# Optimization experiments

Hardware: AMD Instinct MI355X
Metric: run time of the kernel (lower is better)

## Reference

```python
import jax, jax.numpy as jnp
import numpy as np

B, T, N, F_IN = 4, 8, 2048, 16
HID, HEADS, OUT_CH, OUT_FEAT = 128, 4, 64, 14
E = 32768


def _ln(x, g, b, eps=1e-5):
    mu = x.mean(-1, keepdims=True)
    var = ((x - mu) ** 2).mean(-1, keepdims=True)
    return (x - mu) / jnp.sqrt(var + eps) * g + b


def _attn_steps(x, wq, bq, wk, bk, wv, bv, wo, bo):
    # x: [B, S, M, F]; single-head causal attention over axis 1 (the 'steps' axis)
    q = x @ wq + bq
    k = x @ wk + bk
    v = x @ wv + bv
    scale = 1.0 / np.sqrt(q.shape[-1]).astype(np.float32)
    scores = jnp.einsum('bsmh,btmh->bmst', q, k) * scale  # [B,M,S,S]
    S = scores.shape[-1]
    scores = jnp.where(jnp.tril(jnp.ones((S, S), bool)), scores, -jnp.inf)
    a = jax.nn.softmax(scores, axis=-1)
    ctx = jnp.einsum('bmst,btmh->bsmh', a, v)
    return ctx @ wo + bo


def _attn_nodes(x, wq, bq, wk, bk, wv, bv, wo, bo):
    # single-head attention over axis 2 (the 'nodes' axis)
    q = x @ wq + bq
    k = x @ wk + bk
    v = x @ wv + bv
    scale = 1.0 / np.sqrt(q.shape[-1]).astype(np.float32)
    scores = jnp.einsum('bsnh,bsmh->bsnm', q, k) * scale
    a = jax.nn.softmax(scores, axis=-1)
    ctx = jnp.einsum('bsnm,bsmh->bsnh', a, v)
    return ctx @ wo + bo


def _gat(h, src, dst, n, W, a_src, a_dst, bias, heads, out_ch, concat):
    # PyG GATConv: gather src/dst features per edge, segment softmax over
    # incoming edges of each target node, weighted scatter-aggregate.
    hw = (h @ W).reshape(n, heads, out_ch)
    al_s = (hw * a_src).sum(-1)  # [n, heads]
    al_d = (hw * a_dst).sum(-1)
    loop = jnp.arange(n, dtype=src.dtype)
    src_f = jnp.concatenate([src, loop])
    dst_f = jnp.concatenate([dst, loop])
    alpha = jax.nn.leaky_relu(al_s[src_f] + al_d[dst_f], 0.2)
    # PyG removes pre-existing self-loops then adds canonical ones: mask them out.
    drop = jnp.concatenate([src == dst, jnp.zeros((n,), bool)])[:, None]
    amax = jax.lax.stop_gradient(
        jax.ops.segment_max(jnp.where(drop, -jnp.inf, alpha), dst_f, num_segments=n))
    ex = jnp.where(drop, 0.0, jnp.exp(alpha - amax[dst_f]))
    denom = jax.ops.segment_sum(ex, dst_f, num_segments=n)
    w = ex / denom[dst_f]  # [E_total, heads]
    out = jax.ops.segment_sum(hw[src_f] * w[:, :, None], dst_f, num_segments=n)
    if concat:
        return out.reshape(n, heads * out_ch) + bias
    return out.mean(1) + bias


def _forward(x, edge_index, ln1_g, ln1_b, t_wq, t_bq, t_wk, t_bk, t_wv, t_bv, t_wo, t_bo,
             skip_w, skip_b, ln2_g, ln2_b, s_wq, s_bq, s_wk, s_bk, s_wv, s_bv, s_wo, s_bo,
             ln3_g, ln3_b, mlp_w1, mlp_b1, mlp_w2, mlp_b2,
             gat1_w, gat1_asrc, gat1_adst, gat1_b, gat2_w, gat2_asrc, gat2_adst, gat2_b,
             ffn_w, ffn_b):
    Bx, Tx, Nx, _ = x.shape
    h = jnp.transpose(x, (0, 2, 1, 3))  # [B, N(steps), T(nodes), F]
    h = (h @ skip_w + skip_b) + _attn_steps(_ln(h, ln1_g, ln1_b),
                                            t_wq, t_bq, t_wk, t_bk, t_wv, t_bv, t_wo, t_bo)
    h = h + _attn_nodes(_ln(h, ln2_g, ln2_b), s_wq, s_bq, s_wk, s_bk, s_wv, s_bv, s_wo, s_bo)
    z = _ln(h, ln3_g, ln3_b)
    h = h + (jax.nn.relu(z @ mlp_w1 + mlp_b1) @ mlp_w2 + mlp_b2)
    h = h[:, :, -1, :].reshape(Bx * Nx, HID)  # last 'nodes'(=T) slot, flatten graphs
    src, dst = edge_index[0], edge_index[1]
    off = jnp.repeat(jnp.arange(Bx, dtype=src.dtype) * Nx, src.shape[0])
    src_b = jnp.tile(src, Bx) + off
    dst_b = jnp.tile(dst, Bx) + off
    nt = Bx * Nx
    g1 = jax.nn.elu(_gat(h, src_b, dst_b, nt, gat1_w, gat1_asrc, gat1_adst, gat1_b,
                         HEADS, HID // HEADS, True))
    g2 = _gat(g1, src_b, dst_b, nt, gat2_w, gat2_asrc, gat2_adst, gat2_b, 1, OUT_CH, False)
    out = g2.reshape(Bx, Nx, OUT_CH) @ ffn_w + ffn_b
    return jnp.transpose(out, (0, 2, 1))  # [B, output_features, N]


def setup_inputs():
    key = jax.random.key(0)
    ki = iter(list(jax.random.split(key, 40)))
    def rn(shape, s=0.05):
        return jax.random.normal(next(ki), shape, jnp.float32) * s
    d = {}
    d['x'] = jax.random.normal(next(ki), (B, T, N, F_IN), jnp.float32)
    d['edge_index'] = jax.random.randint(next(ki), (2, E), 0, N, jnp.int32)
    d['ln1_g'] = jnp.ones((F_IN,), jnp.float32); d['ln1_b'] = jnp.zeros((F_IN,), jnp.float32)
    d['t_wq'] = rn((F_IN, HID)); d['t_bq'] = jnp.zeros((HID,), jnp.float32)
    d['t_wk'] = rn((F_IN, HID)); d['t_bk'] = jnp.zeros((HID,), jnp.float32)
    d['t_wv'] = rn((F_IN, HID)); d['t_bv'] = jnp.zeros((HID,), jnp.float32)
    d['t_wo'] = rn((HID, HID)); d['t_bo'] = jnp.zeros((HID,), jnp.float32)
    d['skip_w'] = rn((F_IN, HID)); d['skip_b'] = jnp.zeros((HID,), jnp.float32)
    d['ln2_g'] = jnp.ones((HID,), jnp.float32); d['ln2_b'] = jnp.zeros((HID,), jnp.float32)
    d['s_wq'] = rn((HID, HID)); d['s_bq'] = jnp.zeros((HID,), jnp.float32)
    d['s_wk'] = rn((HID, HID)); d['s_bk'] = jnp.zeros((HID,), jnp.float32)
    d['s_wv'] = rn((HID, HID)); d['s_bv'] = jnp.zeros((HID,), jnp.float32)
    d['s_wo'] = rn((HID, HID)); d['s_bo'] = jnp.zeros((HID,), jnp.float32)
    d['ln3_g'] = jnp.ones((HID,), jnp.float32); d['ln3_b'] = jnp.zeros((HID,), jnp.float32)
    d['mlp_w1'] = rn((HID, 2 * HID)); d['mlp_b1'] = jnp.zeros((2 * HID,), jnp.float32)
    d['mlp_w2'] = rn((2 * HID, HID)); d['mlp_b2'] = jnp.zeros((HID,), jnp.float32)
    d['gat1_w'] = rn((HID, HID))
    d['gat1_asrc'] = rn((HEADS, HID // HEADS)); d['gat1_adst'] = rn((HEADS, HID // HEADS))
    d['gat1_b'] = jnp.zeros((HID,), jnp.float32)
    d['gat2_w'] = rn((HID, OUT_CH))
    d['gat2_asrc'] = rn((1, OUT_CH)); d['gat2_adst'] = rn((1, OUT_CH))
    d['gat2_b'] = jnp.zeros((OUT_CH,), jnp.float32)
    d['ffn_w'] = rn((OUT_CH, OUT_FEAT)); d['ffn_b'] = jnp.zeros((OUT_FEAT,), jnp.float32)
    return d


def reference(x, edge_index, ln1_g, ln1_b, t_wq, t_bq, t_wk, t_bk, t_wv, t_bv, t_wo, t_bo,
              skip_w, skip_b, ln2_g, ln2_b, s_wq, s_bq, s_wk, s_bk, s_wv, s_bv, s_wo, s_bo,
              ln3_g, ln3_b, mlp_w1, mlp_b1, mlp_w2, mlp_b2,
              gat1_w, gat1_asrc, gat1_adst, gat1_b, gat2_w, gat2_asrc, gat2_adst, gat2_b,
              ffn_w, ffn_b):
    return _forward(x, edge_index, ln1_g, ln1_b, t_wq, t_bq, t_wk, t_bk, t_wv, t_bv, t_wo, t_bo,
                    skip_w, skip_b, ln2_g, ln2_b, s_wq, s_bq, s_wk, s_bk, s_wv, s_bv, s_wo, s_bo,
                    ln3_g, ln3_b, mlp_w1, mlp_b1, mlp_w2, mlp_b2,
                    gat1_w, gat1_asrc, gat1_adst, gat1_b, gat2_w, gat2_asrc, gat2_adst, gat2_b,
                    ffn_w, ffn_b)
```

## Files before the change

### kernel.cpp

```cpp
#include <hip/hip_runtime.h>
#include <hip/hip_bf16.h>
#include <stdint.h>


#define BB     4
#define TT     8
#define NN     2048
#define FIN    16
#define HID    128
#define BM     (BB*TT)
#define PROWS  (BM*NN)
#define NHEADS 4
#define OUTCH  64
#define OUTF   14
#define NEDGE  32768
#define NEDGEB (NEDGE*BB)
#define NNODE  (BB*NN)
#define NETOT  (NEDGEB + NNODE)

#define TQ     64
#define NTILE  (NN/TQ)

typedef __hip_bfloat16 bf16;
typedef __attribute__((ext_vector_type(8))) short bf16x8;
typedef __attribute__((ext_vector_type(4))) float f32x4;

__device__ __forceinline__ float b2f(bf16 v){ return __bfloat162float(v); }
__device__ __forceinline__ bf16  f2b(float f){ return __float2bfloat16(f); }
__device__ __forceinline__ unsigned short bfbits(float f){
    union { bf16 h; unsigned short u; } cv; cv.h = f2b(f); return cv.u;
}

__global__ __launch_bounds__(256)
void k_kv(const float* __restrict__ x,
          const float* __restrict__ g1, const float* __restrict__ bb1,
          const float* __restrict__ wk, const float* __restrict__ bk,
          const float* __restrict__ wv, const float* __restrict__ bv,
          int in_off, bf16* __restrict__ K, bf16* __restrict__ Vt)
{
    const int r0 = blockIdx.x * 32;
    const int t  = threadIdx.x;

    __shared__ float wk_s[FIN][HID];
    __shared__ float wv_s[FIN][HID];
    __shared__ float xr_s[32][FIN+1];
    __shared__ float ln_s[32][FIN+1];

    #pragma unroll
    for (int it = 0; it < 2; ++it){
        const int u = t + it*256;
        ((float4*)wk_s)[u] = ((const float4*)wk)[u];
        ((float4*)wv_s)[u] = ((const float4*)wv)[u];
    }
    #pragma unroll
    for (int it = 0; it < 2; ++it){
        const int u = t + it*256;
        xr_s[u >> 4][u & 15] = x[(size_t)(r0 + in_off)*FIN + u];
    }
    __syncthreads();

    if (t < 32){
        float mu = 0.f;
        #pragma unroll
        for (int f = 0; f < FIN; ++f) mu += xr_s[t][f];
        mu *= (1.f/FIN);
        float var = 0.f;
        #pragma unroll
        for (int f = 0; f < FIN; ++f){ float d = xr_s[t][f]-mu; var += d*d; }
        var *= (1.f/FIN);
        const float inv = rsqrtf(var + 1e-5f);
        #pragma unroll
        for (int f = 0; f < FIN; ++f)
            ln_s[t][f] = (xr_s[t][f]-mu)*inv*g1[f] + bb1[f];
    }
    __syncthreads();

    {
        const int hk = (t & 63)*2;
        const float2 bkv = *(const float2*)&bk[hk];
        #pragma unroll
        for (int pass = 0; pass < 8; ++pass){
            const int key = pass*4 + (t >> 6);
            float a0 = bkv.x, a1 = bkv.y;
            #pragma unroll
            for (int f = 0; f < FIN; ++f){
                const float l = ln_s[key][f];
                const float2 wkv = ((const float2*)&wk_s[f][0])[t & 63];
                a0 += l*wkv.x; a1 += l*wkv.y;
            }
            const unsigned int pk =
                (unsigned int)bfbits(a0) | ((unsigned int)bfbits(a1) << 16);
            *(unsigned int*)(void*)&K[((size_t)(r0 + key))*HID + hk] = pk;
        }
    }

    {
        const int slice = r0 >> 11;
        const int kg    = (r0 & (NN-1)) >> 5;
        const size_t vbase = ((size_t)slice*(NN/32) + kg)*(size_t)HID*32;
        const int kk = (t & 15)*2;
        #pragma unroll
        for (int pass = 0; pass < 8; ++pass){
            const int h = (t >> 4) + 16*pass;
            float a0 = bv[h], a1 = a0;
            #pragma unroll
            for (int f = 0; f < FIN; ++f){
                const float wvf = wv_s[f][h];
                a0 += ln_s[kk  ][f] * wvf;
                a1 += ln_s[kk+1][f] * wvf;
            }
            const unsigned int pk =
                (unsigned int)bfbits(a0) | ((unsigned int)bfbits(a1) << 16);
            *(unsigned int*)(void*)&Vt[vbase + (size_t)h*32 + kk] = pk;
        }
    }
}

__global__ __launch_bounds__(256)
void k_attn_mfma(const float* __restrict__ x,
                 const bf16* __restrict__ K, const bf16* __restrict__ Vt,
                 const float* __restrict__ g1, const float* __restrict__ bb1,
                 const float* __restrict__ wq, const float* __restrict__ bq,
                 const bf16* __restrict__ BH1,
                 const float* __restrict__ t_bo, const float* __restrict__ skb,
                 int slice_off, bf16* __restrict__ CXH1)
{
    int slice, tile, kvslice;
    if (gridDim.y == 1){
        const int bid = (int)blockIdx.x;
        slice   = (bid & 7)*4 + ((bid >> 3) & 3);
        tile    = (NTILE-1) - (bid >> 5);
        kvslice = slice;
    } else {
        tile    = (NTILE-1) - (int)blockIdx.y;
        slice   = (int)blockIdx.x + slice_off;
        kvslice = (int)blockIdx.x;
    }
    const int q0    = tile*TQ;
    const int t     = threadIdx.x;
    const int w     = t >> 6;
    const int lane  = t & 63;
    const int quad  = lane >> 4;
    const int l16   = lane & 15;
    const int wr0   = w*16;

    const float qscale = 0.08838834764831845f * 1.4426950408889634f;

    __shared__ float xs [TQ][FIN+1];
    __shared__ __align__(16) bf16 SM[12032];
    bf16* Psb = SM;
    bf16* Ks  = SM + 2560;
    bf16* Vs  = SM + 6912;
    bf16 (*wqs)[32] = (bf16(*)[32])(SM + 2560);
    bf16 (*xsb)[32] = (bf16(*)[32])(SM + 6656);
    bf16 (*Qv)[136] = (bf16(*)[136])(SM + 2560);
    bf16* AE  = SM;

    const size_t kb = (size_t)kvslice * NN * HID;
    const size_t vb = (size_t)kvslice * (size_t)(NN/32) * HID*32;
    const bf16* kptr = K  + kb + (size_t)t*8;
    const bf16* vptr = Vt + vb + (size_t)t*8;
    bf16x8 kreg0, kreg1, vreg0, vreg1;
    kreg0 = *(const bf16x8*)(const void*)(kptr);
    kreg1 = *(const bf16x8*)(const void*)(kptr + 2048);
    vreg0 = *(const bf16x8*)(const void*)(vptr);
    vreg1 = *(const bf16x8*)(const void*)(vptr + 2048);

    #pragma unroll
    for (int it = 0; it < 4; ++it){
        const int u = t + it*256;
        xs[u >> 4][u & 15] = x[((size_t)slice*NN + q0)*FIN + u];
    }
    #pragma unroll
    for (int it = 0; it < 8; ++it){
        const int u = t + it*256;
        const int f = u >> 7, ch = u & 127;
        wqs[ch][f] = f2b(wq[u] * qscale);
    }
    {
        const bf16x8 z8 = {0,0,0,0,0,0,0,0};
        const int ch = t >> 1, k0 = 16 + (t & 1)*8;
        *(bf16x8*)(void*)&wqs[ch][k0] = z8;
    }
    __syncthreads();

    if (t < TQ){
        float mu = 0.f;
        #pragma unroll
        for (int f = 0; f < FIN; ++f) mu += xs[t][f];
        mu *= (1.f/FIN);
        float var = 0.f;
        #pragma unroll
        for (int f = 0; f < FIN; ++f){ float d = xs[t][f]-mu; var += d*d; }
        var *= (1.f/FIN);
        const float inv = rsqrtf(var + 1e-5f);
        bf16x8 v0, v1;
        #pragma unroll
        for (int f = 0; f < 8; ++f)
            v0[f] = (short)bfbits((xs[t][f]-mu)*inv*g1[f] + bb1[f]);
        #pragma unroll
        for (int f = 0; f < 8; ++f)
            v1[f] = (short)bfbits((xs[t][8+f]-mu)*inv*g1[8+f] + bb1[8+f]);
        const bf16x8 z8 = {0,0,0,0,0,0,0,0};
        *(bf16x8*)(void*)&xsb[t][0]  = v0;
        *(bf16x8*)(void*)&xsb[t][8]  = v1;
        *(bf16x8*)(void*)&xsb[t][16] = z8;
        *(bf16x8*)(void*)&xsb[t][24] = z8;
    }
    __syncthreads();

    {
        const bf16x8 af = *(const bf16x8*)(const void*)&xsb[wr0 + l16][quad*8];
        f32x4 Cq[8];
        #pragma unroll
        for (int ct = 0; ct < 8; ++ct){
            const bf16x8 bfv = *(const bf16x8*)(const void*)&wqs[ct*16 + l16][quad*8];
            Cq[ct] = __builtin_amdgcn_mfma_f32_16x16x32_bf16(
                         af, bfv, (f32x4){0.f,0.f,0.f,0.f}, 0, 0, 0);
        }
        __syncthreads();
        #pragma unroll
        for (int ct = 0; ct < 8; ++ct){
            const int col = ct*16 + l16;
            const float bqs = bq[col] * qscale;
            #pragma unroll
            for (int r = 0; r < 4; ++r)
                Qv[wr0 + quad*4 + r][col] = f2b(Cq[ct][r] + bqs);
        }
    }
    __syncthreads();

    bf16x8 qf[4];
    #pragma unroll
    for (int ks = 0; ks < 4; ++ks)
        qf[ks] = *(const bf16x8*)(const void*)&Qv[wr0 + l16][ks*32 + quad*8];
    __syncthreads();

    f32x4 O[8];
    #pragma unroll
    for (int ct = 0; ct < 8; ++ct) O[ct] = (f32x4){0.f,0.f,0.f,0.f};
    float l_[4] = {0.f,0.f,0.f,0.f};

    const int jend_blk = q0 + TQ - 1;
    const int my_jmax  = q0 + wr0 + 15;
    const int brow = q0 + wr0 + quad*4;

    bf16* ksA = &Ks[((t      ) >> 4)*136 + ((t      ) & 15)*8];
    bf16* ksB = &Ks[((t + 256) >> 4)*136 + ((t + 256) & 15)*8];
    bf16* vsA = &Vs[((t      ) >> 2)*40  + ((t      ) &  3)*8];
    bf16* vsB = &Vs[((t + 256) >> 2)*40  + ((t + 256) &  3)*8];
    const bf16* kr0 = &Ks[(2*l16    )*136 + quad*8];
    const bf16* kr1 = &Ks[(2*l16 + 1)*136 + quad*8];
    const bf16* vr  = &Vs[l16*40 + quad*8];
    bf16* psw = &Psb[w*640 + (quad*4)*40 + 2*l16];
    const bf16* psr = &Psb[w*640 + l16*40 + quad*8];

    for (int j0 = 0; j0 <= jend_blk; j0 += 32){
        *(bf16x8*)(void*)ksA = kreg0;
        *(bf16x8*)(void*)ksB = kreg1;
        *(bf16x8*)(void*)vsA = vreg0;
        *(bf16x8*)(void*)vsB = vreg1;
        __syncthreads();

        if (j0 + 32 <= jend_blk){
            const size_t off = (size_t)(j0 + 32)*128;
            kreg0 = *(const bf16x8*)(const void*)(kptr + off);
            kreg1 = *(const bf16x8*)(const void*)(kptr + off + 2048);
            vreg0 = *(const bf16x8*)(const void*)(vptr + off);
            vreg1 = *(const bf16x8*)(const void*)(vptr + off + 2048);
        }

        if (j0 <= my_jmax){
            f32x4 S0 = (f32x4){0.f,0.f,0.f,0.f}, S1 = S0;
            #pragma unroll
            for (int ks = 0; ks < 4; ++ks){
                const bf16x8 kf0 = *(const bf16x8*)(const void*)(kr0 + ks*32);
                const bf16x8 kf1 = *(const bf16x8*)(const void*)(kr1 + ks*32);
                S0 = __builtin_amdgcn_mfma_f32_16x16x32_bf16(qf[ks], kf0, S0, 0, 0, 0);
                S1 = __builtin_amdgcn_mfma_f32_16x16x32_bf16(qf[ks], kf1, S1, 0, 0, 0);
            }
            float sv0[4], sv1[4];
            if (j0 + 31 > q0 + wr0){
                const int c0j = j0 + 2*l16, c1j = c0j + 1;
                #pragma unroll
                for (int r = 0; r < 4; ++r){
                    sv0[r] = (c0j <= brow + r) ? S0[r] : -1e30f;
                    sv1[r] = (c1j <= brow + r) ? S1[r] : -1e30f;
                }
            } else {
                #pragma unroll
                for (int r = 0; r < 4; ++r){ sv0[r] = S0[r]; sv1[r] = S1[r]; }
            }
            #pragma unroll
            for (int r = 0; r < 4; ++r){
                const float e0 = __builtin_amdgcn_exp2f(sv0[r]);
                const float e1 = __builtin_amdgcn_exp2f(sv1[r]);
                l_[r] += e0 + e1;
                const unsigned int pk =
                    (unsigned int)bfbits(e0) | ((unsigned int)bfbits(e1) << 16);
                *(unsigned int*)(void*)(psw + r*40) = pk;
            }
            const bf16x8 pf = *(const bf16x8*)(const void*)psr;
            #pragma unroll
            for (int ct = 0; ct < 8; ++ct){
                const bf16x8 vf = *(const bf16x8*)(const void*)(vr + ct*16*40);
                O[ct] = __builtin_amdgcn_mfma_f32_16x16x32_bf16(pf, vf, O[ct], 0, 0, 0);
            }
        }
        __syncthreads();
    }

    {
        float inv[4];
        #pragma unroll
        for (int r = 0; r < 4; ++r){
            float rs = l_[r];
            rs += __shfl_xor(rs, 1);
            rs += __shfl_xor(rs, 2);
            rs += __shfl_xor(rs, 4);
            rs += __shfl_xor(rs, 8);
            inv[r] = 1.f/rs;
        }
        #pragma unroll
        for (int ct = 0; ct < 8; ++ct)
        #pragma unroll
        for (int r = 0; r < 4; ++r)
            AE[(wr0 + quad*4 + r)*168 + ct*16 + l16] = f2b(O[ct][r]*inv[r]);
    }
    #pragma unroll
    for (int it = 0; it < 4; ++it){
        const int u = t + it*256;
        AE[(u >> 4)*168 + 128 + (u & 15)] = f2b(xs[u >> 4][u & 15]);
    }
    #pragma unroll
    for (int it = 0; it < 6; ++it){
        const int u = t + it*256;
        const int row = u/24;
        AE[row*168 + 144 + (u - row*24)] = f2b(0.f);
    }
    __syncthreads();

    f32x4 O2[8];
    #pragma unroll
    for (int ct = 0; ct < 8; ++ct) O2[ct] = (f32x4){0.f,0.f,0.f,0.f};
    #pragma unroll
    for (int k5 = 0; k5 < 5; ++k5){
        const bf16x8 af = *(const bf16x8*)(const void*)
            &AE[(wr0 + l16)*168 + k5*32 + quad*8];
        #pragma unroll
        for (int ct = 0; ct < 8; ++ct){
            const bf16x8 bfv = *(const bf16x8*)(const void*)
                (BH1 + (size_t)(ct*16 + l16)*168 + k5*32 + quad*8);
            O2[ct] = __builtin_amdgcn_mfma_f32_16x16x32_bf16(af, bfv, O2[ct], 0, 0, 0);
        }
    }
    __syncthreads();
    #pragma unroll
    for (int ct = 0; ct < 8; ++ct){
        const int col = ct*16 + l16;
        const float bias = t_bo[col] + skb[col];
        #pragma unroll
        for (int r = 0; r < 4; ++r)
            AE[(wr0 + quad*4 + r)*168 + col] = f2b(O2[ct][r] + bias);
    }
    __syncthreads();
    {
        const int row = t >> 2, ch0 = (t & 3)*32;
        bf16* dst = CXH1 + ((size_t)slice*NN + q0 + row)*HID + ch0;
        #pragma unroll
        for (int c = 0; c < 4; ++c)
            *(bf16x8*)(void*)(dst + c*8) =
                *(const bf16x8*)(const void*)&AE[row*168 + ch0 + c*8];
    }
}

__global__ __launch_bounds__(256)
void k_prep(const float* __restrict__ s_wq, const float* __restrict__ s_wk,
            const float* __restrict__ bq, const float* __restrict__ bk,
            const float* __restrict__ s_wv, const float* __restrict__ s_wo,
            const float* __restrict__ g1w, const float* __restrict__ w1,
            const float* __restrict__ w2,
            const float* __restrict__ t_wo, const float* __restrict__ skw,
            bf16* __restrict__ Mt, bf16* __restrict__ wvT, bf16* __restrict__ woT,
            bf16* __restrict__ g1wT, bf16* __restrict__ w1T, bf16* __restrict__ w2T,
            bf16* __restrict__ BH1,
            float* __restrict__ vk, float* __restrict__ vq, float* __restrict__ sbb)
{
    const int b = blockIdx.x;
    const int t = threadIdx.x;
    __shared__ float wq_s[HID*HID];
    __shared__ float wk_s[8][HID];
    if (b < 16){
        for (int u = t; u < HID*HID; u += 256) wq_s[u] = s_wq[u];
        for (int u = t; u < 8*HID;   u += 256) ((float*)wk_s)[u] = s_wk[b*8*HID + u];
        __syncthreads();
        #pragma unroll
        for (int i = 0; i < 4; ++i){
            const int e = t + i*256;
            const int cl = e >> 7, a = e & 127;
            float acc = 0.f;
            for (int hh = 0; hh < HID; ++hh) acc += wk_s[cl][hh]*wq_s[a*HID + hh];
            Mt[(size_t)(b*8 + cl)*HID + a] = f2b(acc);
        }
    } else if (b == 16){
        if (t < HID){
            float a1 = 0.f, a2 = 0.f;
            for (int hh = 0; hh < HID; ++hh){
                a1 += bq[hh]*s_wk[t*HID + hh];
                a2 += s_wq[t*HID + hh]*bk[hh];
            }
            vk[t] = a1; vq[t] = a2;
            if (t == 0){
                float s = 0.f;
                for (int hh = 0; hh < HID; ++hh) s += bq[hh]*bk[hh];
                *sbb = s;
            }
        }
    } else if (b == 17){
        for (int u = t; u < HID*HID; u += 256){
            const int c = u >> 7, h = u & 127;
            wvT[h*HID + c] = f2b(s_wv[u]);
        }
    } else if (b == 18){
        for (int u = t; u < HID*HID; u += 256){
            const int c = u >> 7, h = u & 127;
            woT[h*HID + c] = f2b(s_wo[u]);
        }
    } else if (b == 19){
        for (int u = t; u < HID*HID; u += 256){
            const int c = u >> 7, h = u & 127;
            g1wT[h*HID + c] = f2b(g1w[u]);
        }
    } else if (b == 20){
        for (int u = t; u < HID*2*HID; u += 256){
            const int k = u >> 8, n = u & 255;
            w1T[n*HID + k] = f2b(w1[u]);
        }
    } else if (b == 21){
        for (int u = t; u < 2*HID*HID; u += 256){
            const int k = u >> 7, n = u & 127;
            w2T[(size_t)n*2*HID + k] = f2b(w2[u]);
        }
    } else if (b == 22){
        for (int u = t; u < HID*168; u += 256){
            const int c = u / 168, k = u - c*168;
            float v = 0.f;
            if (k < 128)      v = t_wo[k*HID + c];
            else if (k < 144) v = skw[(k-128)*HID + c];
            BH1[u] = f2b(v);
        }
    }
}

__global__ __launch_bounds__(256)
void k_mix(const bf16* __restrict__ H1,
           const float* __restrict__ ln2g, const float* __restrict__ ln2b,
           const bf16* __restrict__ Mt, const bf16* __restrict__ wvT,
           const bf16* __restrict__ woT, const bf16* __restrict__ g1wT,
           const bf16* __restrict__ w1T, const bf16* __restrict__ w2T,
           const float* __restrict__ vk, const float* __restrict__ vq,
           const float* __restrict__ sbbp,
           const float* __restrict__ s_bv, const float* __restrict__ s_bo,
           const float* __restrict__ bm1, const float* __restrict__ bm2,
           const float* __restrict__ ln3g, const float* __restrict__ ln3b,
           const float* __restrict__ g1as, const float* __restrict__ g1ad,
           bf16* __restrict__ hw1, float* __restrict__ als1, float* __restrict__ ald1)
{
    const int blk0 = blockIdx.x * 16;
    const int bb = blk0 >> 11, s0 = blk0 & (NN-1);
    const int t = threadIdx.x;
    const int w = t >> 6;
    const int lane = t & 63;
    const int quad = lane >> 4;
    const int l16  = lane & 15;

    __shared__ bf16  h1s[16][TT][136];
    __shared__ bf16  ZA [16][136];
    __shared__ bf16  HLs[16][264];
    __shared__ float Cw [16][128];
    __shared__ float ln2gs[HID], ln2bs[HID];
    __shared__ float mu_s[16][TT], inv_s[16][TT];
    __shared__ float ps[16][TT];
    __shared__ float sbq_s[16], mu3[16], inv3[16];

    for (int m = 0; m < TT; ++m){
        const bf16* src = H1 + ((size_t)(bb*TT + m)*NN + s0)*HID;
        const int node = t >> 4, c8 = t & 15;
        *(bf16x8*)(void*)&h1s[node][m][c8*8] =
            *(const bf16x8*)(const void*)(src + (size_t)node*HID + c8*8);
    }
    if (t < HID){ ln2gs[t] = ln2g[t]; ln2bs[t] = ln2b[t]; }
    __syncthreads();

    {
        const int idx = t >> 1, half = t & 1;
        const int node = idx >> 3, m = idx & 7;
        float sum = 0.f, sq = 0.f;
        for (int c = half; c < HID; c += 2){
            const float v = b2f(h1s[node][m][c]);
            sum += v; sq += v*v;
        }
        sum += __shfl_xor(sum, 1); sq += __shfl_xor(sq, 1);
        if (half == 0){
            const float mu = sum*(1.f/HID);
            const float var = sq*(1.f/HID) - mu*mu;
            mu_s[node][m] = mu;
            inv_s[node][m] = rsqrtf(var + 1e-5f);
        }
    }
    __syncthreads();

    #pragma unroll
    for (int i = 0; i < 8; ++i){
        const int idx = t + i*256;
        const int n = idx >> 7, c = idx & 127;
        const float z = (b2f(h1s[n][7][c]) - mu_s[n][7])*inv_s[n][7]*ln2gs[c] + ln2bs[c];
        ZA[n][c] = f2b(z);
    }
    if (t < 128){
        const int node = t >> 3, l8 = t & 7;
        float sp = 0.f;
        for (int c = l8; c < HID; c += 8){
            const float z = (b2f(h1s[node][7][c]) - mu_s[node][7])*inv_s[node][7]*ln2gs[c] + ln2bs[c];
            sp += vq[c]*z;
        }
        sp += __shfl_xor(sp, 1);
        sp += __shfl_xor(sp, 2);
        sp += __shfl_xor(sp, 4);
        if (l8 == 0) sbq_s[node] = sp;
    }
    __syncthreads();

    {
        bf16x8 af[4];
        #pragma unroll
        for (int ks = 0; ks < 4; ++ks)
            af[ks] = *(const bf16x8*)(const void*)&ZA[l16][ks*32 + quad*8];
        __syncthreads();
        f32x4 C0 = (f32x4){0,0,0,0}, C1 = C0;
        #pragma unroll
        for (int ks = 0; ks < 4; ++ks){
            const bf16x8 b0 = *(const bf16x8*)(const void*)(Mt + (size_t)(w*32      + l16)*HID + ks*32 + quad*8);
            const bf16x8 b1 = *(const bf16x8*)(const void*)(Mt + (size_t)(w*32 + 16 + l16)*HID + ks*32 + quad*8);
            C0 = __builtin_amdgcn_mfma_f32_16x16x32_bf16(af[ks], b0, C0, 0, 0, 0);
            C1 = __builtin_amdgcn_mfma_f32_16x16x32_bf16(af[ks], b1, C1, 0, 0, 0);
        }
        const int c0 = w*32 + l16, c1 = c0 + 16;
        #pragma unroll
        for (int r = 0; r < 4; ++r){
            Cw[quad*4 + r][c0] = C0[r] + vk[c0];
            Cw[quad*4 + r][c1] = C1[r] + vk[c1];
        }
    }
    __syncthreads();

    {
        const int idx = t >> 1, half = t & 1;
        const int node = idx >> 3, m = idx & 7;
        const float mu = mu_s[node][m], iv = inv_s[node][m];
        float d = 0.f;
        for (int c = half; c < HID; c += 2){
            const float z = (b2f(h1s[node][m][c]) - mu)*iv*ln2gs[c] + ln2bs[c];
            d += Cw[node][c]*z;
        }
        d += __shfl_xor(d, 1);
        if (half == 0)
            ps[node][m] = (d + sbq_s[node] + *sbbp) * 0.08838834764831845f;
    }
    __syncthreads();
    if (t < 16){
        float mx = -1e30f;
        #pragma unroll
        for (int m = 0; m < TT; ++m) mx = fmaxf(mx, ps[t][m]);
        float p[TT], se = 0.f;
        #pragma unroll
        for (int m = 0; m < TT; ++m){ p[m] = __expf(ps[t][m]-mx); se += p[m]; }
        const float isum = 1.f/se;
        #pragma unroll
        for (int m = 0; m < TT; ++m) ps[t][m] = p[m]*isum;
    }
    __syncthreads();
    #pragma unroll
    for (int i = 0; i < 8; ++i){
        const int idx = t + i*256;
        const int n = idx >> 7, c = idx & 127;
        const float gc = ln2gs[c], bc = ln2bs[c];
        float acc = 0.f;
        #pragma unroll
        for (int m = 0; m < TT; ++m){
            const float z = (b2f(h1s[n][m][c]) - mu_s[n][m])*inv_s[n][m]*gc + bc;
            acc += ps[n][m]*z;
        }
        ZA[n][c] = f2b(acc);
    }
    __syncthreads();

    {
        bf16x8 af[4];
        #pragma unroll
        for (int ks = 0; ks < 4; ++ks)
            af[ks] = *(const bf16x8*)(const void*)&ZA[l16][ks*32 + quad*8];
        __syncthreads();
        f32x4 C0 = (f32x4){0,0,0,0}, C1 = C0;
        #pragma unroll
        for (int ks = 0; ks < 4; ++ks){
            const bf16x8 b0 = *(const bf16x8*)(const void*)(wvT + (size_t)(w*32      + l16)*HID + ks*32 + quad*8);
            const bf16x8 b1 = *(const bf16x8*)(const void*)(wvT + (size_t)(w*32 + 16 + l16)*HID + ks*32 + quad*8);
            C0 = __builtin_amdgcn_mfma_f32_16x16x32_bf16(af[ks], b0, C0, 0, 0, 0);
            C1 = __builtin_amdgcn_mfma_f32_16x16x32_bf16(af[ks], b1, C1, 0, 0, 0);
        }
        const int c0 = w*32 + l16, c1 = c0 + 16;
        #pragma unroll
        for (int r = 0; r < 4; ++r){
            ZA[quad*4 + r][c0] = f2b(C0[r] + s_bv[c0]);
            ZA[quad*4 + r][c1] = f2b(C1[r] + s_bv[c1]);
        }
    }
    __syncthreads();

    {
        bf16x8 af[4];
        #pragma unroll
        for (int ks = 0; ks < 4; ++ks)
            af[ks] = *(const bf16x8*)(const void*)&ZA[l16][ks*32 + quad*8];
        __syncthreads();
        f32x4 C0 = (f32x4){0,0,0,0}, C1 = C0;
        #pragma unroll
        for (int ks = 0; ks < 4; ++ks){
            const bf16x8 b0 = *(const bf16x8*)(const void*)(woT + (size_t)(w*32      + l16)*HID + ks*32 + quad*8);
            const bf16x8 b1 = *(const bf16x8*)(const void*)(woT + (size_t)(w*32 + 16 + l16)*HID + ks*32 + quad*8);
            C0 = __builtin_amdgcn_mfma_f32_16x16x32_bf16(af[ks], b0, C0, 0, 0, 0);
            C1 = __builtin_amdgcn_mfma_f32_16x16x32_bf16(af[ks], b1, C1, 0, 0, 0);
        }
        const int c0 = w*32 + l16, c1 = c0 + 16;
        #pragma unroll
        for (int r = 0; r < 4; ++r){
            const int node = quad*4 + r;
            Cw[node][c0] = C0[r] + s_bo[c0] + b2f(h1s[node][7][c0]);
            Cw[node][c1] = C1[r] + s_bo[c1] + b2f(h1s[node][7][c1]);
        }
    }
    __syncthreads();

    {
        const int node = t >> 4, part = t & 15;
        float sum = 0.f, sq = 0.f;
        for (int c = part; c < HID; c += 16){
            const float v = Cw[node][c];
            sum += v; sq += v*v;
        }
        sum += __shfl_xor(sum, 1); sq += __shfl_xor(sq, 1);
        sum += __shfl_xor(sum, 2); sq += __shfl_xor(sq, 2);
        sum += __shfl_xor(sum, 4); sq += __shfl_xor(sq, 4);
        sum += __shfl_xor(sum, 8); sq += __shfl_xor(sq, 8);
        if (part == 0){
            const float mu = sum*(1.f/HID);
            const float var = sq*(1.f/HID) - mu*mu;
            mu3[node] = mu;
            inv3[node] = rsqrtf(var + 1e-5f);
        }
    }
    __syncthreads();
    #pragma unroll
    for (int i = 0; i < 8; ++i){
        const int idx = t + i*256;
        const int n = idx >> 7, c = idx & 127;
        ZA[n][c] = f2b((Cw[n][c] - mu3[n])*inv3[n]*ln3g[c] + ln3b[c]);
    }
    __syncthreads();

    {
        bf16x8 af[4];
        #pragma unroll
        for (int ks = 0; ks < 4; ++ks)
            af[ks] = *(const bf16x8*)(const void*)&ZA[l16][ks*32 + quad*8];
        __syncthreads();
        f32x4 C[4];
        #pragma unroll
        for (int u = 0; u < 4; ++u) C[u] = (f32x4){0,0,0,0};
        #pragma unroll
        for (int ks = 0; ks < 4; ++ks){
            #pragma unroll
            for (int u = 0; u < 4; ++u){
                const bf16x8 bfv = *(const bf16x8*)(const void*)
                    (w1T + (size_t)(w*64 + u*16 + l16)*HID + ks*32 + quad*8);
                C[u] = __builtin_amdgcn_mfma_f32_16x16x32_bf16(af[ks], bfv, C[u], 0, 0, 0);
            }
        }
        #pragma unroll
        for (int u = 0; u < 4; ++u){
            const int col = w*64 + u*16 + l16;
            const float bias = bm1[col];
            #pragma unroll
            for (int r = 0; r < 4; ++r)
                HLs[quad*4 + r][col] = f2b(fmaxf(C[u][r] + bias, 0.f));
        }
    }
    __syncthreads();

    {
        bf16x8 af[8];
        #pragma unroll
        for (int ks = 0; ks < 8; ++ks)
            af[ks] = *(const bf16x8*)(const void*)&HLs[l16][ks*32 + quad*8];
        __syncthreads();
        f32x4 C0 = (f32x4){0,0,0,0}, C1 = C0;
        #pragma unroll
        for (int ks = 0; ks < 8; ++ks){
            const bf16x8 b0 = *(const bf16x8*)(const void*)(w2T + (size_t)(w*32      + l16)*2*HID + ks*32 + quad*8);
            const bf16x8 b1 = *(const bf16x8*)(const void*)(w2T + (size_t)(w*32 + 16 + l16)*2*HID + ks*32 + quad*8);
            C0 = __builtin_amdgcn_mfma_f32_16x16x32_bf16(af[ks], b0, C0, 0, 0, 0);
            C1 = __builtin_amdgcn_mfma_f32_16x16x32_bf16(af[ks], b1, C1, 0, 0, 0);
        }
        const int c0 = w*32 + l16, c1 = c0 + 16;
        #pragma unroll
        for (int r = 0; r < 4; ++r){
            const int node = quad*4 + r;
            ZA[node][c0] = f2b(C0[r] + bm2[c0] + Cw[node][c0]);
            ZA[node][c1] = f2b(C1[r] + bm2[c1] + Cw[node][c1]);
        }
    }
    __syncthreads();

    {
        bf16x8 af[4];
        #pragma unroll
        for (int ks = 0; ks < 4; ++ks)
            af[ks] = *(const bf16x8*)(const void*)&ZA[l16][ks*32 + quad*8];
        __syncthreads();
        f32x4 C0 = (f32x4){0,0,0,0}, C1 = C0;
        #pragma unroll
        for (int ks = 0; ks < 4; ++ks){
            const bf16x8 b0 = *(const bf16x8*)(const void*)(g1wT + (size_t)(w*32      + l16)*HID + ks*32 + quad*8);
            const bf16x8 b1 = *(const bf16x8*)(const void*)(g1wT + (size_t)(w*32 + 16 + l16)*HID + ks*32 + quad*8);
            C0 = __builtin_amdgcn_mfma_f32_16x16x32_bf16(af[ks], b0, C0, 0, 0, 0);
            C1 = __builtin_amdgcn_mfma_f32_16x16x32_bf16(af[ks], b1, C1, 0, 0, 0);
        }
        const int c0 = w*32 + l16, c1 = c0 + 16;
        #pragma unroll
        for (int r = 0; r < 4; ++r){
            Cw[quad*4 + r][c0] = C0[r];
            Cw[quad*4 + r][c1] = C1[r];
        }
    }
    __syncthreads();

    #pragma unroll
    for (int i = 0; i < 8; ++i){
        const int idx = t + i*256;
        hw1[(size_t)blk0*HID + idx] = f2b(((const float*)Cw)[idx]);
    }
    if (t < 64){
        const int node = t >> 2, hd = t & 3;
        float s1 = 0.f, s2 = 0.f;
        for (int j = 0; j < 32; ++j){
            const int c = hd*32 + j;
            const float a = Cw[node][c];
            s1 += a*g1as[c];
            s2 += a*g1ad[c];
        }
        als1[(blk0 + node)*NHEADS + hd] = s1;
        ald1[(blk0 + node)*NHEADS + hd] = s2;
    }
}

__global__ void k_csr_hist(const int* __restrict__ ei, int* __restrict__ cnt)
{
    const int e = blockIdx.x*blockDim.x + threadIdx.x;
    if (e >= NEDGE) return;
    const int s = ei[e], d = ei[NEDGE + e];
    if (s != d) atomicAdd(&cnt[d], 1);
}

__global__ __launch_bounds__(256)
void k_csr_scan(const int* __restrict__ cnt, int* __restrict__ roff)
{
    const int t = threadIdx.x;
    __shared__ int part[256];
    int loc[8]; int s = 0;
    #pragma unroll
    for (int i = 0; i < 8; ++i){ loc[i] = s; s += cnt[t*8 + i]; }
    part[t] = s;
    __syncthreads();
    if (t == 0){
        int acc = 0;
        for (int i = 0; i < 256; ++i){ const int v = part[i]; part[i] = acc; acc += v; }
    }
    __syncthreads();
    const int base_ = part[t];
    #pragma unroll
    for (int i = 0; i < 8; ++i) roff[t*8 + i] = base_ + loc[i];
    if (t == 255) roff[2048] = base_ + s;
}

__global__ void k_csr_scatter(const int* __restrict__ ei, const int* __restrict__ roff,
                              int* __restrict__ fill, int* __restrict__ col)
{
    const int e = blockIdx.x*blockDim.x + threadIdx.x;
    if (e >= NEDGE) return;
    const int s = ei[e], d = ei[NEDGE + e];
    if (s != d){
        const int p = roff[d] + atomicAdd(&fill[d], 1);
        col[p] = s;
    }
}

__global__ __launch_bounds__(64)
void k_gat_g1lin(const int* __restrict__ roff, const int* __restrict__ col,
                 const float* __restrict__ als, const float* __restrict__ ald,
                 const bf16* __restrict__ hw, const float* __restrict__ g1b,
                 const float* __restrict__ W,
                 const float* __restrict__ asrc, const float* __restrict__ adst,
                 bf16* __restrict__ hw2, float* __restrict__ al2s, float* __restrict__ al2d)
{
    const int nid = blockIdx.x;
    const int d   = nid & (NN-1);
    const int gb  = nid & ~(NN-1);
    const int c2  = threadIdx.x;
    const int hd  = c2 >> 4;
    const float ad = ald[nid*NHEADS + hd];

    float av0 = 0.f, av1 = 0.f, accd = 0.f;
    const int e0 = roff[d], e1 = roff[d+1];
    int sn = (e0 < e1) ? col[e0] : 0;
    for (int e = e0; e < e1; ++e){
        const int s = sn + gb;
        sn = (e+1 < e1) ? col[e+1] : 0;
        float a = als[s*NHEADS + hd] + ad;
        a = a > 0.f ? a : 0.2f*a;
        const float ex = __expf(a);
        const unsigned int pk =
            *(const unsigned int*)(const void*)&hw[(size_t)s*HID + 2*c2];
        av0 += ex * __uint_as_float(pk << 16);
        av1 += ex * __uint_as_float(pk & 0xffff0000u);
        accd += ex;
    }
    {
        float a = als[nid*NHEADS + hd] + ad;
        a = a > 0.f ? a : 0.2f*a;
        const float ex = __expf(a);
        const unsigned int pk =
            *(const unsigned int*)(const void*)&hw[(size_t)nid*HID + 2*c2];
        av0 += ex * __uint_as_float(pk << 16);
        av1 += ex * __uint_as_float(pk & 0xffff0000u);
        accd += ex;
    }
    __shared__ float hrs[HID];
    {
        float v0 = av0/accd + g1b[2*c2];
        float v1 = av1/accd + g1b[2*c2+1];
        v0 = v0 > 0.f ? v0 : expm1f(v0);
        v1 = v1 > 0.f ? v1 : expm1f(v1);
        *(float2*)(void*)&hrs[2*c2] = make_float2(v0, v1);
    }
    __syncthreads();

    const int c = c2;
    float a = 0.f;
    for (int k = 0; k < HID; ++k) a += hrs[k]*W[k*OUTCH + c];
    hw2[(size_t)nid*OUTCH + c] = f2b(a);
    float s1 = a*asrc[c], s2 = a*adst[c];
    #pragma unroll
    for (int off = 32; off > 0; off >>= 1){
        s1 += __shfl_down(s1, off);
        s2 += __shfl_down(s2, off);
    }
    if (c == 0){ al2s[nid] = s1; al2d[nid] = s2; }
}

__global__ __launch_bounds__(64)
void k_gat_gather2f(const int* __restrict__ roff, const int* __restrict__ col,
                    const float* __restrict__ als, const float* __restrict__ ald,
                    const bf16* __restrict__ hw2, const float* __restrict__ g2b,
                    const float* __restrict__ fw, const float* __restrict__ fb,
                    float* __restrict__ out)
{
    const int nid = blockIdx.x;
    const int d   = nid & (NN-1);
    const int gb  = nid & ~(NN-1);
    const int c   = threadIdx.x;
    const float ad = ald[nid];

    float accv = 0.f, accd = 0.f;
    const int e0 = roff[d], e1 = roff[d+1];
    int sn = (e0 < e1) ? col[e0] : 0;
    for (int e = e0; e < e1; ++e){
        const int s = sn + gb;
        sn = (e+1 < e1) ? col[e+1] : 0;
        float a = als[s] + ad;
        a = a > 0.f ? a : 0.2f*a;
        const float ex = __expf(a);
        accv += ex * b2f(hw2[(size_t)s*OUTCH + c]);
        accd += ex;
    }
    {
        float a = als[nid] + ad;
        a = a > 0.f ? a : 0.2f*a;
        const float ex = __expf(a);
        accv += ex * b2f(hw2[(size_t)nid*OUTCH + c]);
        accd += ex;
    }
    __shared__ float g[OUTCH];
    g[c] = accv/accd + g2b[c];
    __syncthreads();
    if (c < OUTF){
        float o = fb[c];
        #pragma unroll
        for (int k = 0; k < OUTCH; ++k) o += g[k]*fw[k*OUTF + c];
        const int b = nid >> 11, n = nid & (NN-1);
        out[((size_t)b*OUTF + c)*NN + n] = o;
    }
}

extern "C" void kernel_launch(void* const* d_in, const int* in_sizes, int n_in,
                              void* d_out, int out_size, void* d_ws, size_t ws_size,
                              hipStream_t stream)
{
    const float* x    = (const float*)d_in[0];
    const int*  ei    = (const int*)d_in[1];
    const float* ln1g = (const float*)d_in[2];  const float* ln1b = (const float*)d_in[3];
    const float* t_wq = (const float*)d_in[4];  const float* t_bq = (const float*)d_in[5];
    const float* t_wk = (const float*)d_in[6];  const float* t_bk = (const float*)d_in[7];
    const float* t_wv = (const float*)d_in[8];  const float* t_bv = (const float*)d_in[9];
    const float* t_wo = (const float*)d_in[10]; const float* t_bo = (const float*)d_in[11];
    const float* skw  = (const float*)d_in[12]; const float* skb  = (const float*)d_in[13];
    const float* ln2g = (const float*)d_in[14]; const float* ln2b = (const float*)d_in[15];
    const float* s_wq = (const float*)d_in[16]; const float* s_bq = (const float*)d_in[17];
    const float* s_wk = (const float*)d_in[18]; const float* s_bk = (const float*)d_in[19];
    const float* s_wv = (const float*)d_in[20]; const float* s_bv = (const float*)d_in[21];
    const float* s_wo = (const float*)d_in[22]; const float* s_bo = (const float*)d_in[23];
    const float* ln3g = (const float*)d_in[24]; const float* ln3b = (const float*)d_in[25];
    const float* w1   = (const float*)d_in[26]; const float* b1   = (const float*)d_in[27];
    const float* w2   = (const float*)d_in[28]; const float* b2   = (const float*)d_in[29];
    const float* g1w  = (const float*)d_in[30];
    const float* g1as = (const float*)d_in[31]; const float* g1ad = (const float*)d_in[32];
    const float* g1b  = (const float*)d_in[33];
    const float* g2w  = (const float*)d_in[34];
    const float* g2as = (const float*)d_in[35]; const float* g2ad = (const float*)d_in[36];
    const float* g2b  = (const float*)d_in[37];
    const float* ffw  = (const float*)d_in[38]; const float* ffb  = (const float*)d_in[39];
    float* out = (float*)d_out;

    const size_t MiB = 1024u*1024u;
    const bool wide = ws_size >= 48*MiB;

    char* base = (char*)d_ws;
    bf16 *Kb, *Vtb, *CXH1;
    char* gat_base;
    if (wide){
        Kb   = (bf16*)(base + 0*MiB);
        Vtb  = (bf16*)(base + 16*MiB);
        CXH1 = (bf16*)(base + 32*MiB);
        gat_base = base;
    } else {
        CXH1 = (bf16*)(base + 0*MiB);
        gat_base = base + 16*MiB;
        Kb   = (bf16*)(base + 26*MiB);
        Vtb  = (bf16*)(base + 26*MiB + 512u*1024u);
    }

    char* ob = (char*)d_out;
    bf16*  Mt   = (bf16*)(ob);
    bf16*  wvT  = (bf16*)(ob + 32*1024);
    bf16*  woT  = (bf16*)(ob + 64*1024);
    bf16*  g1wT = (bf16*)(ob + 96*1024);
    bf16*  w1T  = (bf16*)(ob + 128*1024);
    bf16*  w2T  = (bf16*)(ob + 192*1024);
    float* vkw  = (float*)(ob + 256*1024);
    float* vqw  = (float*)(ob + 256*1024 + 512);
    float* sbb  = (float*)(ob + 256*1024 + 1024);
    bf16*  BH1  = (bf16*)(ob + 272*1024);

    char* w = gat_base;
    auto alloc = [&](size_t bytes){ void* p = (void*)w; w += (bytes + 255) & ~(size_t)255; return p; };
    int*   cnt  = (int*)  alloc(2048u*sizeof(int));
    int*   fill = (int*)  alloc(2048u*sizeof(int));
    int*   roff = (int*)  alloc(2049u*sizeof(int));
    int*   col  = (int*)  alloc((size_t)NEDGE*sizeof(int));
    bf16*  hw1  = (bf16*) alloc((size_t)NNODE*HID*sizeof(bf16));
    float* als1 = (float*)alloc((size_t)NNODE*NHEADS*sizeof(float));
    float* ald1 = (float*)alloc((size_t)NNODE*NHEADS*sizeof(float));
    bf16*  hw2  = (bf16*) alloc((size_t)NNODE*OUTCH*sizeof(bf16));
    float* als2 = (float*)alloc((size_t)NNODE*sizeof(float));
    float* ald2 = (float*)alloc((size_t)NNODE*sizeof(float));

    k_prep<<<32, 256, 0, stream>>>(s_wq, s_wk, s_bq, s_bk, s_wv, s_wo, g1w, w1, w2,
                                   t_wo, skw,
                                   Mt, wvT, woT, g1wT, w1T, w2T, BH1,
                                   vkw, vqw, sbb);
    if (wide){
        k_kv<<<PROWS/32, 256, 0, stream>>>(x, ln1g, ln1b, t_wk, t_bk, t_wv, t_bv, 0, Kb, Vtb);
        k_attn_mfma<<<BM*NTILE, 256, 0, stream>>>(x, Kb, Vtb, ln1g, ln1b,
                                                  t_wq, t_bq, BH1, t_bo, skb, 0, CXH1);
    } else {
        for (int s = 0; s < BM; ++s){
            k_kv<<<NN/32, 256, 0, stream>>>(x, ln1g, ln1b, t_wk, t_bk, t_wv, t_bv, s*NN, Kb, Vtb);
            k_attn_mfma<<<dim3(1, NTILE), 256, 0, stream>>>(x, Kb, Vtb, ln1g, ln1b,
                                                            t_wq, t_bq, BH1, t_bo, skb, s, CXH1);
        }
    }

    hipMemsetAsync(cnt, 0, 2u*2048u*sizeof(int), stream);
    k_csr_hist   <<<NEDGE/256, 256, 0, stream>>>(ei, cnt);
    k_csr_scan   <<<1,        256, 0, stream>>>(cnt, roff);
    k_csr_scatter<<<NEDGE/256, 256, 0, stream>>>(ei, roff, fill, col);

    k_mix<<<NNODE/16, 256, 0, stream>>>(CXH1, ln2g, ln2b, Mt, wvT, woT, g1wT, w1T, w2T,
                                        vkw, vqw, sbb, s_bv, s_bo, b1, b2,
                                        ln3g, ln3b, g1as, g1ad, hw1, als1, ald1);

    k_gat_g1lin  <<<NNODE, 64, 0, stream>>>(roff, col, als1, ald1, hw1, g1b,
                                            g2w, g2as, g2ad, hw2, als2, ald2);
    k_gat_gather2f<<<NNODE, 64, 0, stream>>>(roff, col, als2, ald2, hw2, g2b, ffw, ffb, out);
}
```

Measured before the change: 387.2 us.

## Fuse CSR build into one LDS-atomic kernel and vectorize k_mix LDS reads

Replaces the memset plus three CSR kernels (histogram, scan, scatter) with a single 1024-thread block that counts, scans and scatters using shared-memory atomics. This removes three launches and the global atomics. Separately, the layernorm statistics, score dot-product and weighted-sum loops in k_mix now read eight bf16 values per LDS access and convert bits directly, and write ZA as one 16-byte vector. The cost is that one block serially processes all 32768 edges twice on a single CU, and the vector reads may change LDS bank-conflict patterns.

```diff
diff --git a/kernel.cpp b/kernel.cpp
--- a/kernel.cpp
+++ b/kernel.cpp
@@ -29,6 +29,9 @@
 __device__ __forceinline__ bf16  f2b(float f){ return __float2bfloat16(f); }
 __device__ __forceinline__ unsigned short bfbits(float f){
     union { bf16 h; unsigned short u; } cv; cv.h = f2b(f); return cv.u;
+}
+__device__ __forceinline__ float bu2f(unsigned short u){
+    union { unsigned int i; float f; } c; c.i = ((unsigned int)u) << 16; return c.f;
 }
 
 __global__ __launch_bounds__(256)
@@ -496,9 +499,14 @@
         const int idx = t >> 1, half = t & 1;
         const int node = idx >> 3, m = idx & 7;
         float sum = 0.f, sq = 0.f;
-        for (int c = half; c < HID; c += 2){
-            const float v = b2f(h1s[node][m][c]);
-            sum += v; sq += v*v;
+        #pragma unroll
+        for (int j = 0; j < 8; ++j){
+            const bf16x8 v = *(const bf16x8*)(const void*)&h1s[node][m][half*64 + j*8];
+            #pragma unroll
+            for (int e = 0; e < 8; ++e){
+                const float f = bu2f((unsigned short)v[e]);
+                sum += f; sq += f*f;
+            }
         }
         sum += __shfl_xor(sum, 1); sq += __shfl_xor(sq, 1);
         if (half == 0){
@@ -559,9 +567,15 @@
         const int node = idx >> 3, m = idx & 7;
         const float mu = mu_s[node][m], iv = inv_s[node][m];
         float d = 0.f;
-        for (int c = half; c < HID; c += 2){
-            const float z = (b2f(h1s[node][m][c]) - mu)*iv*ln2gs[c] + ln2bs[c];
-            d += Cw[node][c]*z;
+        #pragma unroll
+        for (int j = 0; j < 8; ++j){
+            const int cb = half*64 + j*8;
+            const bf16x8 v = *(const bf16x8*)(const void*)&h1s[node][m][cb];
+            #pragma unroll
+            for (int e = 0; e < 8; ++e){
+                const float z = (bu2f((unsigned short)v[e]) - mu)*iv*ln2gs[cb+e] + ln2bs[cb+e];
+                d += Cw[node][cb+e]*z;
+            }
         }
         d += __shfl_xor(d, 1);
         if (half == 0)
@@ -580,18 +594,24 @@
         for (int m = 0; m < TT; ++m) ps[t][m] = p[m]*isum;
     }
     __syncthreads();
-    #pragma unroll
-    for (int i = 0; i < 8; ++i){
-        const int idx = t + i*256;
-        const int n = idx >> 7, c = idx & 127;
-        const float gc = ln2gs[c], bc = ln2bs[c];
-        float acc = 0.f;
+    {
+        const int n = t >> 4, c0 = (t & 15)*8;
+        float acc[8] = {0.f,0.f,0.f,0.f,0.f,0.f,0.f,0.f};
         #pragma unroll
         for (int m = 0; m < TT; ++m){
-            const float z = (b2f(h1s[n][m][c]) - mu_s[n][m])*inv_s[n][m]*gc + bc;
-            acc += ps[n][m]*z;
-        }
-        ZA[n][c] = f2b(acc);
+            const float pm = ps[n][m];
+            const float mu = mu_s[n][m], iv = inv_s[n][m];
+            const bf16x8 v = *(const bf16x8*)(const void*)&h1s[n][m][c0];
+            #pragma unroll
+            for (int e = 0; e < 8; ++e){
+                const float z = (bu2f((unsigned short)v[e]) - mu)*iv*ln2gs[c0+e] + ln2bs[c0+e];
+                acc[e] += pm*z;
+            }
+        }
+        bf16x8 o;
+        #pragma unroll
+        for (int e = 0; e < 8; ++e) o[e] = (short)bfbits(acc[e]);
+        *(bf16x8*)(void*)&ZA[n][c0] = o;
     }
     __syncthreads();
 
@@ -764,44 +784,47 @@
     }
 }
 
-__global__ void k_csr_hist(const int* __restrict__ ei, int* __restrict__ cnt)
+__global__ __launch_bounds__(1024)
+void k_csr(const int* __restrict__ ei, int* __restrict__ roff, int* __restrict__ col)
 {
-    const int e = blockIdx.x*blockDim.x + threadIdx.x;
-    if (e >= NEDGE) return;
-    const int s = ei[e], d = ei[NEDGE + e];
-    if (s != d) atomicAdd(&cnt[d], 1);
-}
-
-__global__ __launch_bounds__(256)
-void k_csr_scan(const int* __restrict__ cnt, int* __restrict__ roff)
-{
+    __shared__ int cntL[2048];
+    __shared__ int part[256];
     const int t = threadIdx.x;
-    __shared__ int part[256];
-    int loc[8]; int s = 0;
-    #pragma unroll
-    for (int i = 0; i < 8; ++i){ loc[i] = s; s += cnt[t*8 + i]; }
-    part[t] = s;
+    for (int u = t; u < 2048; u += 1024) cntL[u] = 0;
+    __syncthreads();
+    for (int e = t; e < NEDGE; e += 1024){
+        const int s = ei[e], d = ei[NEDGE + e];
+        if (s != d) atomicAdd(&cntL[d], 1);
+    }
+    __syncthreads();
+    int loc[8]; int msum = 0;
+    if (t < 256){
+        #pragma unroll
+        for (int i = 0; i < 8; ++i){ loc[i] = msum; msum += cntL[t*8 + i]; }
+        part[t] = msum;
+    }
     __syncthreads();
     if (t == 0){
         int acc = 0;
         for (int i = 0; i < 256; ++i){ const int v = part[i]; part[i] = acc; acc += v; }
     }
     __syncthreads();
-    const int base_ = part[t];
-    #pragma unroll
-    for (int i = 0; i < 8; ++i) roff[t*8 + i] = base_ + loc[i];
-    if (t == 255) roff[2048] = base_ + s;
-}
-
-__global__ void k_csr_scatter(const int* __restrict__ ei, const int* __restrict__ roff,
-                              int* __restrict__ fill, int* __restrict__ col)
-{
-    const int e = blockIdx.x*blockDim.x + threadIdx.x;
-    if (e >= NEDGE) return;
-    const int s = ei[e], d = ei[NEDGE + e];
-    if (s != d){
-        const int p = roff[d] + atomicAdd(&fill[d], 1);
-        col[p] = s;
+    if (t < 256){
+        const int b = part[t];
+        #pragma unroll
+        for (int i = 0; i < 8; ++i){
+            roff[t*8 + i] = b + loc[i];
+            cntL[t*8 + i] = b + loc[i];
+        }
+        if (t == 255) roff[2048] = b + msum;
+    }
+    __syncthreads();
+    for (int e = t; e < NEDGE; e += 1024){
+        const int s = ei[e], d = ei[NEDGE + e];
+        if (s != d){
+            const int p = atomicAdd(&cntL[d], 1);
+            col[p] = s;
+        }
     }
 }
 
@@ -973,8 +996,6 @@
 
     char* w = gat_base;
     auto alloc = [&](size_t bytes){ void* p = (void*)w; w += (bytes + 255) & ~(size_t)255; return p; };
-    int*   cnt  = (int*)  alloc(2048u*sizeof(int));
-    int*   fill = (int*)  alloc(2048u*sizeof(int));
     int*   roff = (int*)  alloc(2049u*sizeof(int));
     int*   col  = (int*)  alloc((size_t)NEDGE*sizeof(int));
     bf16*  hw1  = (bf16*) alloc((size_t)NNODE*HID*sizeof(bf16));
@@ -1000,10 +1021,7 @@
         }
     }
 
-    hipMemsetAsync(cnt, 0, 2u*2048u*sizeof(int), stream);
-    k_csr_hist   <<<NEDGE/256, 256, 0, stream>>>(ei, cnt);
-    k_csr_scan   <<<1,        256, 0, stream>>>(cnt, roff);
-    k_csr_scatter<<<NEDGE/256, 256, 0, stream>>>(ei, roff, fill, col);
+    k_csr<<<1, 1024, 0, stream>>>(ei, roff, col);
 
     k_mix<<<NNODE/16, 256, 0, stream>>>(CXH1, ln2g, ln2b, Mt, wvT, woT, g1wT, w1T, w2T,
                                         vkw, vqw, sbb, s_bv, s_bo, b1, b2,
```

After: 398.0 us. 1.03x slower.
